# Kernel tuning notes

Measured on AMD Instinct MI355X. Metric: run time of the kernel, lower is better.

The kernel has to match this reference:

```python
import jax, jax.numpy as jnp
import numpy as np

B, T, N, F, C, H, O = 4, 8, 4096, 32, 32, 64, 1
RADIUS = 50.0   # adjacency_threshold on pairwise distance
EPS = 1e-5      # batchnorm eps


def setup_inputs() -> dict:
    key = jax.random.key(0)
    ks = jax.random.split(key, 8)
    x = jax.random.normal(ks[0], (B, T, N, F), jnp.float32)
    # dist_mat from random 2D node locations in a 1000x1000 area; avg degree ~32
    loc = jax.random.uniform(ks[1], (N, 2), jnp.float32) * 1000.0
    d2 = jnp.sum((loc[:, None, :] - loc[None, :, :]) ** 2, axis=-1)  # [N,N]
    adj = (d2 < RADIUS ** 2).astype(jnp.float32)                     # includes self (d=0)
    dinv = 1.0 / jnp.sqrt(jnp.maximum(adj.sum(-1), 1.0))
    adj_norm = adj * dinv[:, None] * dinv[None, :]                   # D^-1/2 A D^-1/2
    s = 0.05
    return dict(
        x=x,
        adj_norm=adj_norm,
        bn_gamma=jnp.ones((F,), jnp.float32),
        bn_beta=jnp.zeros((F,), jnp.float32),
        W_gcn=jax.random.normal(ks[2], (F, C), jnp.float32) * s,
        b_gcn=jnp.zeros((C,), jnp.float32),
        W_ih=jax.random.normal(ks[3], (C, 3 * H), jnp.float32) * s,
        W_hh=jax.random.normal(ks[4], (H, 3 * H), jnp.float32) * s,
        b_ih=jnp.zeros((3 * H,), jnp.float32),
        b_hh=jnp.zeros((3 * H,), jnp.float32),
        W_dense=jax.random.normal(ks[5], (H, O), jnp.float32) * s,
        b_dense=jnp.zeros((O,), jnp.float32),
    )


def reference(x, adj_norm, bn_gamma, bn_beta, W_gcn, b_gcn, W_ih, W_hh, b_ih, b_hh, W_dense, b_dense):
    # BatchNorm2d over feature channel (training-mode batch stats, biased var)
    mean = x.mean(axis=(0, 1, 2))
    var = x.var(axis=(0, 1, 2))
    xn = (x - mean) * jax.lax.rsqrt(var + EPS) * bn_gamma + bn_beta  # [B,T,N,F]
    # GCN association (same math every timestep -> batch over T)
    ya = jnp.einsum('mn,btnf->btmf', adj_norm, xn)                   # neighbor aggregate
    y = jnp.einsum('btnf,fc->btnc', ya, W_gcn) + b_gcn               # [B,T,N,C]
    # precompute input-gate projections, then scan GRU cell over time
    gi = jnp.einsum('btnc,ch->btnh', y, W_ih) + b_ih                 # [B,T,N,3H]
    gi = jnp.transpose(gi, (1, 0, 2, 3))                             # [T,B,N,3H]

    def step(h, g):
        gh = h @ W_hh + b_hh
        r = jax.nn.sigmoid(g[..., :H] + gh[..., :H])
        z = jax.nn.sigmoid(g[..., H:2 * H] + gh[..., H:2 * H])
        n = jnp.tanh(g[..., 2 * H:] + r * gh[..., 2 * H:])
        h_new = (1.0 - z) * n + z * h
        return h_new, h_new

    h0 = jnp.zeros((B, N, H), x.dtype)
    _, hs = jax.lax.scan(step, h0, gi)                               # [T,B,N,H]
    out = jnp.transpose(hs, (1, 0, 2, 3)) @ W_dense + b_dense        # [B,T,N,O]
    return out
```

## Files before the change

kernel.cpp:

```cpp
#include <hip/hip_runtime.h>
#include <hip/hip_bf16.h>
#include <stdint.h>

#define B_ 4
#define T_ 8
#define N_ 4096
#define F_ 32
#define BT_ (B_*T_)
#define ROWS_ (B_*N_)
#define CAP_ 128
#define EPS_ 1e-5f
#define NELEM_ (B_*T_*N_*F_)

#define WS_BNS    0
#define WS_ROWSUM 16384
#define WS_DEG    (WS_ROWSUM + 4096)
#define WS_FRG    (WS_DEG + 4096)
#define WS_PAIR   (WS_FRG + 52*256)
#define WS_XA     (WS_PAIR + 4096*CAP_*2)

typedef float v4f __attribute__((ext_vector_type(4)));
typedef _Float16 half8 __attribute__((ext_vector_type(8)));
union HU { uint32_t u[4]; half8 v; };

__device__ inline float sigm_f(float x) {
  return __builtin_amdgcn_rcpf(1.0f + __expf(-x));
}
__device__ inline uint32_t f16pair(float a, float b) {
  union { _Float16 h; unsigned short s; } x, y;
  x.h = (_Float16)a; y.h = (_Float16)b;
  return (uint32_t)x.s | ((uint32_t)y.s << 16);
}
__device__ inline void sp2(float a0, float a1, uint32_t& hi, uint32_t& lo) {
  _Float16 h0 = (_Float16)a0, h1 = (_Float16)a1;
  float r0 = a0 - (float)h0, r1 = a1 - (float)h1;
  union { _Float16 h; unsigned short s; } u0, u1, v0, v1;
  u0.h = h0; u1.h = h1; v0.h = (_Float16)r0; v1.h = (_Float16)r1;
  hi = (uint32_t)u0.s | ((uint32_t)u1.s << 16);
  lo = (uint32_t)v0.s | ((uint32_t)v1.s << 16);
}

__global__ void __launch_bounds__(256)
k_pre(const float* __restrict__ x, const float* __restrict__ A, float* __restrict__ ws) {
  if (blockIdx.x < 4096) {
    int m = blockIdx.x;
    __shared__ int cnt;
    __shared__ float wsum[4];
    if (threadIdx.x == 0) cnt = 0;
    __syncthreads();
    int* deg = (int*)&ws[WS_DEG];
    float2* pair = (float2*)&ws[WS_PAIR];
    const float4* A4 = (const float4*)(A + (size_t)m * N_);
    float4 av4[4];
#pragma unroll
    for (int i = 0; i < 4; i++) av4[i] = A4[threadIdx.x + 256 * i];
    float lsum = 0.f;
#pragma unroll
    for (int i = 0; i < 4; i++) {
      float av[4] = {av4[i].x, av4[i].y, av4[i].z, av4[i].w};
      int nb4 = (threadIdx.x + 256 * i) * 4;
#pragma unroll
      for (int r = 0; r < 4; r++) {
        float a = av[r];
        if (a != 0.0f) {
          int p = atomicAdd(&cnt, 1);
          if (p < CAP_) pair[(size_t)m * CAP_ + p] = make_float2(__int_as_float((nb4 + r) * F_), a);
          lsum += a;
        }
      }
    }
#pragma unroll
    for (int off = 32; off > 0; off >>= 1) lsum += __shfl_xor(lsum, off, 64);
    if ((threadIdx.x & 63) == 0) wsum[threadIdx.x >> 6] = lsum;
    __syncthreads();
    int c = cnt;
    for (int p = c + threadIdx.x; p < 68; p += 256)
      pair[(size_t)m * CAP_ + p] = make_float2(__int_as_float(0), 0.0f);
    if (threadIdx.x == 0) {
      deg[m] = min(c, CAP_);
      ws[WS_ROWSUM + m] = wsum[0] + wsum[1] + wsum[2] + wsum[3];
    }
  } else {
    int bnb = blockIdx.x - 4096;
    const float4* x4 = (const float4*)x;
    int tid = bnb * 256 + threadIdx.x;
    float s[4] = {0,0,0,0}, s2[4] = {0,0,0,0};
    for (int i = tid; i < NELEM_ / 4; i += 256 * 256) {
      float4 v = x4[i];
      s[0] += v.x; s2[0] += v.x * v.x;
      s[1] += v.y; s2[1] += v.y * v.y;
      s[2] += v.z; s2[2] += v.z * v.z;
      s[3] += v.w; s2[3] += v.w * v.w;
    }
    __shared__ float ls[256][4], ls2[256][4];
#pragma unroll
    for (int r = 0; r < 4; r++) { ls[threadIdx.x][r] = s[r]; ls2[threadIdx.x][r] = s2[r]; }
    __syncthreads();
    int t = threadIdx.x;
    if (t < 32) {
      int g = t >> 2, r = t & 3;
      float a = 0.f;
      for (int q = g; q < 256; q += 8) a += ls[q][r];
      atomicAdd(&ws[WS_BNS + t], a);
    } else if (t < 64) {
      int cch = t - 32;
      int g = cch >> 2, r = cch & 3;
      float b2 = 0.f;
      for (int q = g; q < 256; q += 8) b2 += ls2[q][r];
      atomicAdd(&ws[WS_BNS + t], b2);
    }
  }
}

__global__ void __launch_bounds__(256)
k_fold(const float* __restrict__ gamma, const float* __restrict__ beta,
       const float* __restrict__ Wg, const float* __restrict__ bg,
       const float* __restrict__ Wih, const float* __restrict__ bih,
       const float* __restrict__ Whh, const float* __restrict__ bhh,
       float* __restrict__ ws) {
  __shared__ float fb[26144];
  float* Wx_s  = fb;
  float* Wih_s = fb + 6144;
  float* Whh_s = fb + 12288;
  float* Wg_s  = fb + 24576;
  float* Us_s  = fb + 25600;
  float* Vs_s  = fb + 25792;
  float* bns   = fb + 25984;
  float* scale_s = fb + 26048;
  float* shift_s = fb + 26080;
  float* p_s   = fb + 26112;
  int tid = threadIdx.x;
#pragma unroll
  for (int i = tid; i < 1536; i += 256) ((float4*)Wih_s)[i] = ((const float4*)Wih)[i];
#pragma unroll
  for (int i = tid; i < 3072; i += 256) ((float4*)Whh_s)[i] = ((const float4*)Whh)[i];
  if (tid < 256) { ((float4*)Wg_s)[tid] = ((const float4*)Wg)[tid]; }
  if (tid < 64) bns[tid] = ws[WS_BNS + tid];
  __syncthreads();
  if (tid < 32) {
    float cntf = (float)(B_ * T_ * N_);
    float mean = bns[tid] / cntf;
    float var = bns[32 + tid] / cntf - mean * mean;
    float sc = gamma[tid] * rsqrtf(var + EPS_);
    scale_s[tid] = sc;
    shift_s[tid] = beta[tid] - mean * sc;
  }
  __syncthreads();
  if (tid < 32) {
    float acc = 0.f;
    for (int f = 0; f < 32; f++) acc += shift_s[f] * Wg_s[f * 32 + tid];
    p_s[tid] = acc;
  }
  __syncthreads();
  for (int e = tid; e < 32 * 192; e += 256) {
    int f = e / 192, j = e % 192;
    float acc = 0.f;
#pragma unroll
    for (int c = 0; c < 32; c++) acc += Wg_s[f * 32 + c] * Wih_s[c * 192 + j];
    Wx_s[e] = scale_s[f] * acc;
  }
  if (tid < 192) {
    float au = 0.f, av = 0.f;
#pragma unroll
    for (int c = 0; c < 32; c++) { au += p_s[c] * Wih_s[c * 192 + tid]; av += bg[c] * Wih_s[c * 192 + tid]; }
    Us_s[tid] = au; Vs_s[tid] = av + bih[tid];
  }
  __syncthreads();
  int w = tid >> 6, L = tid & 63, q = L >> 4, c = L & 15;
  uint32_t* wsu = (uint32_t*)ws;
  for (int fi = w; fi < 52; fi += 4) {
    int mt, kt;
    if (fi < 32)      { mt = fi >> 2;            kt = fi & 3; }
    else if (fi < 40) { mt = 8 + ((fi - 32) >> 1); kt = (fi & 1) ? 3 : 0; }
    else              { int r = fi - 40; mt = 12 + r / 3; kt = 1 + r % 3; }
    int cls = mt >> 2;
    int col = (cls < 2) ? mt * 16 + c : 128 + (mt & 3) * 16 + c;
#pragma unroll
    for (int d = 0; d < 4; d++) {
      float a01[2];
#pragma unroll
      for (int h2 = 0; h2 < 2; h2++) {
        int k = kt * 32 + q * 8 + 2 * d + h2;
        float v;
        if (k < 32)       v = (cls == 3) ? 0.f : Wx_s[k * 192 + col];
        else if (k < 96)  v = (cls == 2) ? 0.f : Whh_s[(k - 32) * 192 + col];
        else if (k == 96) v = (cls == 3) ? 0.f : Us_s[col];
        else if (k == 97) v = (cls < 2) ? (Vs_s[col] + bhh[col]) : (cls == 2 ? Vs_s[col] : bhh[col]);
        else              v = 0.f;
        a01[h2] = v;
      }
      wsu[WS_FRG + fi * 256 + L * 4 + d] = f16pair(a01[0], a01[1]);
    }
  }
}

#define AGG_STEP(d) { \
    float vv = pv[d]; \
    v4f t0 = pb0[d], t1 = pb1[d]; \
    float2 p = pl[row * 69 + k + 4 + d]; \
    int off = __float_as_int(p.x) + fo; \
    pv[d] = p.y; \
    pb0[d] = *(const v4f*)(xb0 + off); \
    pb1[d] = *(const v4f*)(xb1 + off); \
    acc0 += vv * t0; acc1 += vv * t1; }

__global__ void __launch_bounds__(256, 8)
k_agg(const float* __restrict__ x, float* __restrict__ ws) {
  __shared__ float2 pl[32 * 69];
  int tid = threadIdx.x;
  int chunk = blockIdx.x & 15;
  int mg = blockIdx.x >> 4;
  int row = tid >> 3, f4 = tid & 7;
  int m = mg * 32 + row;
  const int* deg = (const int*)&ws[WS_DEG];
  const float2* pair = (const float2*)&ws[WS_PAIR];
  for (int qq = tid; qq < 32 * 68; qq += 256) {
    int r = qq / 68, sl = qq - r * 68;
    pl[r * 69 + sl] = pair[(size_t)(mg * 32 + r) * CAP_ + sl];
  }
  __syncthreads();
  int d0 = deg[m];
  int dm = min(d0, 64);
  int bound = dm;
  bound = max(bound, __shfl_xor(bound, 8, 64));
  bound = max(bound, __shfl_xor(bound, 16, 64));
  bound = max(bound, __shfl_xor(bound, 32, 64));
  bound = (bound + 3) & ~3;
  int bt0 = chunk * 2;
  const float* xb0 = x + (size_t)bt0 * N_ * F_;
  const float* xb1 = xb0 + N_ * F_;
  int fo = f4 * 4;
  v4f acc0 = {0,0,0,0}, acc1 = {0,0,0,0};
  v4f pb0[4], pb1[4];
  float pv[4];
#pragma unroll
  for (int d = 0; d < 4; d++) {
    float2 p = pl[row * 69 + d];
    int off = __float_as_int(p.x) + fo;
    pv[d] = p.y;
    pb0[d] = *(const v4f*)(xb0 + off);
    pb1[d] = *(const v4f*)(xb1 + off);
  }
  for (int k = 0; k < bound; k += 4) {
    AGG_STEP(0) AGG_STEP(1) AGG_STEP(2) AGG_STEP(3)
  }
  if (d0 > 64) {
    for (int k = 64; k < d0; k++) {
      float2 p = pair[(size_t)m * CAP_ + k];
      int off = __float_as_int(p.x) + fo;
      float vv = p.y;
      acc0 += vv * *(const v4f*)(xb0 + off);
      acc1 += vv * *(const v4f*)(xb1 + off);
    }
  }
  size_t ob = (size_t)bt0 * N_ * F_ + m * F_ + fo;
  *(v4f*)(ws + WS_XA + ob) = acc0;
  *(v4f*)(ws + WS_XA + ob + (size_t)N_ * F_) = acc1;
}

#define LDA(fi) (*(const half8*)(frg + (fi)*256 + L*4))
#define DO1(mt, fi, BH, BL) { half8 af = LDA(fi); \
  acc[mt] = __builtin_amdgcn_mfma_f32_16x16x32_f16(af, BH, acc[mt], 0, 0, 0); \
  acc[mt] = __builtin_amdgcn_mfma_f32_16x16x32_f16(af, BL, acc[mt], 0, 0, 0); }

__global__ void __launch_bounds__(256, 1)
k_gru(const float* __restrict__ Wd, const float* __restrict__ bd,
      const float* __restrict__ ws, float* __restrict__ out) {
  __shared__ uint32_t frg[52 * 256];
  __shared__ uint32_t hx[4 * 1344];
  {
    const uint4* gf = (const uint4*)(ws + WS_FRG);
    uint4* sf = (uint4*)frg;
    for (int i = threadIdx.x; i < 52 * 64; i += 256) sf[i] = gf[i];
  }
  __syncthreads();
  int wid = threadIdx.x >> 6, L = threadIdx.x & 63;
  int q = L >> 4, c = L & 15;
  uint32_t* hxw = hx + wid * 1344;
  int row0 = blockIdx.x * 64 + wid * 16;
  int b = row0 >> 12;
  int nb = row0 & (N_ - 1);
  float wdv[4][4];
#pragma unroll
  for (int g = 0; g < 4; g++)
#pragma unroll
    for (int r = 0; r < 4; r++) wdv[g][r] = Wd[16 * g + 4 * q + r];
  float bdv = bd[0];
  HU b3h, b3l;
#pragma unroll
  for (int d = 0; d < 4; d++) { b3h.u[d] = 0; b3l.u[d] = 0; }
  {
    float rsv = ws[WS_ROWSUM + nb + c];
    uint32_t rhi, rlo;
    sp2(rsv, 1.0f, rhi, rlo);
    if (q == 0) { b3h.u[0] = rhi; b3l.u[0] = rlo & 0xFFFFu; }
  }
  float h[4][4];
#pragma unroll
  for (int g = 0; g < 4; g++)
#pragma unroll
    for (int r = 0; r < 4; r++) h[g][r] = 0.f;

  const float* xab = ws + WS_XA;
  size_t xo0 = ((size_t)(b * T_) * N_ + nb + c) * F_ + q * 8;
  float4 xaA = *(const float4*)(xab + xo0);
  float4 xaB = *(const float4*)(xab + xo0 + 4);

  for (int t = 0; t < T_; t++) {
    float4 nxA, nxB;
    if (t < T_ - 1) {
      size_t xo = ((size_t)(b * T_ + t + 1) * N_ + nb + c) * F_ + q * 8;
      nxA = *(const float4*)(xab + xo);
      nxB = *(const float4*)(xab + xo + 4);
    }
#pragma unroll
    for (int g = 0; g < 4; g++)
#pragma unroll
      for (int rp = 0; rp < 2; rp++) {
        uint32_t phi, plo;
        sp2(h[g][2 * rp], h[g][2 * rp + 1], phi, plo);
        int pidx = 8 * g + 2 * q + rp;
        hxw[(pidx * 2 + 0) * 21 + c] = phi;
        hxw[(pidx * 2 + 1) * 21 + c] = plo;
      }
    HU b1h, b1l, b2h, b2l;
#pragma unroll
    for (int d = 0; d < 4; d++) {
      b1h.u[d] = hxw[((4 * q + d) * 2 + 0) * 21 + c];
      b1l.u[d] = hxw[((4 * q + d) * 2 + 1) * 21 + c];
      b2h.u[d] = hxw[((16 + 4 * q + d) * 2 + 0) * 21 + c];
      b2l.u[d] = hxw[((16 + 4 * q + d) * 2 + 1) * 21 + c];
    }
    v4f acc[16];
#pragma unroll
    for (int i = 0; i < 16; i++) acc[i] = (v4f){0.f, 0.f, 0.f, 0.f};
    DO1(0,1,b1h.v,b1l.v)  DO1(1,5,b1h.v,b1l.v)  DO1(2,9,b1h.v,b1l.v)  DO1(3,13,b1h.v,b1l.v)
    DO1(4,17,b1h.v,b1l.v) DO1(5,21,b1h.v,b1l.v) DO1(6,25,b1h.v,b1l.v) DO1(7,29,b1h.v,b1l.v)
    DO1(12,40,b1h.v,b1l.v) DO1(13,43,b1h.v,b1l.v) DO1(14,46,b1h.v,b1l.v) DO1(15,49,b1h.v,b1l.v)
    DO1(0,2,b2h.v,b2l.v)  DO1(1,6,b2h.v,b2l.v)  DO1(2,10,b2h.v,b2l.v) DO1(3,14,b2h.v,b2l.v)
    DO1(4,18,b2h.v,b2l.v) DO1(5,22,b2h.v,b2l.v) DO1(6,26,b2h.v,b2l.v) DO1(7,30,b2h.v,b2l.v)
    DO1(12,41,b2h.v,b2l.v) DO1(13,44,b2h.v,b2l.v) DO1(14,47,b2h.v,b2l.v) DO1(15,50,b2h.v,b2l.v)
    DO1(0,3,b3h.v,b3l.v)  DO1(1,7,b3h.v,b3l.v)  DO1(2,11,b3h.v,b3l.v) DO1(3,15,b3h.v,b3l.v)
    DO1(4,19,b3h.v,b3l.v) DO1(5,23,b3h.v,b3l.v) DO1(6,27,b3h.v,b3l.v) DO1(7,31,b3h.v,b3l.v)
    DO1(8,33,b3h.v,b3l.v) DO1(9,35,b3h.v,b3l.v) DO1(10,37,b3h.v,b3l.v) DO1(11,39,b3h.v,b3l.v)
    DO1(12,42,b3h.v,b3l.v) DO1(13,45,b3h.v,b3l.v) DO1(14,48,b3h.v,b3l.v) DO1(15,51,b3h.v,b3l.v)
    HU b0h, b0l;
    sp2(xaA.x, xaA.y, b0h.u[0], b0l.u[0]);
    sp2(xaA.z, xaA.w, b0h.u[1], b0l.u[1]);
    sp2(xaB.x, xaB.y, b0h.u[2], b0l.u[2]);
    sp2(xaB.z, xaB.w, b0h.u[3], b0l.u[3]);
    DO1(0,0,b0h.v,b0l.v)  DO1(1,4,b0h.v,b0l.v)  DO1(2,8,b0h.v,b0l.v)  DO1(3,12,b0h.v,b0l.v)
    DO1(4,16,b0h.v,b0l.v) DO1(5,20,b0h.v,b0l.v) DO1(6,24,b0h.v,b0l.v) DO1(7,28,b0h.v,b0l.v)
    DO1(8,32,b0h.v,b0l.v) DO1(9,34,b0h.v,b0l.v) DO1(10,36,b0h.v,b0l.v) DO1(11,38,b0h.v,b0l.v)
    float o = 0.f;
#pragma unroll
    for (int g = 0; g < 4; g++)
#pragma unroll
      for (int r = 0; r < 4; r++) {
        float rr = sigm_f(acc[g][r]);
        float z  = sigm_f(acc[4 + g][r]);
        float nn = 2.0f * sigm_f(2.0f * (acc[8 + g][r] + rr * acc[12 + g][r])) - 1.0f;
        float hn = z * (h[g][r] - nn) + nn;
        h[g][r] = hn;
        o += wdv[g][r] * hn;
      }
    o += __shfl_xor(o, 16, 64);
    o += __shfl_xor(o, 32, 64);
    if (L < 16) out[(size_t)(b * T_ + t) * N_ + nb + L] = o + bdv;
    xaA = nxA; xaB = nxB;
  }
}

extern "C" void kernel_launch(void* const* d_in, const int* in_sizes, int n_in,
                              void* d_out, int out_size, void* d_ws, size_t ws_size,
                              hipStream_t stream) {
  const float* x     = (const float*)d_in[0];
  const float* adj   = (const float*)d_in[1];
  const float* gamma = (const float*)d_in[2];
  const float* beta  = (const float*)d_in[3];
  const float* Wg    = (const float*)d_in[4];
  const float* bg    = (const float*)d_in[5];
  const float* Wih   = (const float*)d_in[6];
  const float* Whh   = (const float*)d_in[7];
  const float* bih   = (const float*)d_in[8];
  const float* bhh   = (const float*)d_in[9];
  const float* Wd    = (const float*)d_in[10];
  const float* bd    = (const float*)d_in[11];
  float* ws = (float*)d_ws;
  float* out = (float*)d_out;

  hipMemsetAsync(ws + WS_BNS, 0, 64 * sizeof(float), stream);
  k_pre<<<4096 + 256, 256, 0, stream>>>(x, adj, ws);
  k_fold<<<1, 256, 0, stream>>>(gamma, beta, Wg, bg, Wih, bih, Whh, bhh, ws);
  k_agg<<<2048, 256, 0, stream>>>(x, ws);
  k_gru<<<256, 256, 0, stream>>>(Wd, bd, ws, out);
}
```

Baseline: 206.9 us.

## Fuse sparse neighbor aggregation into GRU kernel via shared memory

Removes the separate aggregation kernel and computes the neighbor-aggregated features for each block's 64 rows across all 8 timesteps directly inside the GRU kernel, keeping them in LDS. This avoids writing and re-reading the aggregated tensor through global memory and saves a kernel launch. In exchange, the gather now runs with only 256 blocks and one block per CU, so far fewer waves are available to hide the latency of the irregular loads. The neighbor-list buffer shares LDS with the hidden-state staging through a union.

```diff
diff --git a/kernel.cpp b/kernel.cpp
--- a/kernel.cpp
+++ b/kernel.cpp
@@ -17,7 +17,6 @@
 #define WS_DEG    (WS_ROWSUM + 4096)
 #define WS_FRG    (WS_DEG + 4096)
 #define WS_PAIR   (WS_FRG + 52*256)
-#define WS_XA     (WS_PAIR + 4096*CAP_*2)
 
 typedef float v4f __attribute__((ext_vector_type(4)));
 typedef _Float16 half8 __attribute__((ext_vector_type(8)));
@@ -194,92 +193,97 @@
   }
 }
 
-#define AGG_STEP(d) { \
-    float vv = pv[d]; \
-    v4f t0 = pb0[d], t1 = pb1[d]; \
-    float2 p = pl[row * 69 + k + 4 + d]; \
-    int off = __float_as_int(p.x) + fo; \
-    pv[d] = p.y; \
-    pb0[d] = *(const v4f*)(xb0 + off); \
-    pb1[d] = *(const v4f*)(xb1 + off); \
-    acc0 += vv * t0; acc1 += vv * t1; }
-
-__global__ void __launch_bounds__(256, 8)
-k_agg(const float* __restrict__ x, float* __restrict__ ws) {
-  __shared__ float2 pl[32 * 69];
-  int tid = threadIdx.x;
-  int chunk = blockIdx.x & 15;
-  int mg = blockIdx.x >> 4;
-  int row = tid >> 3, f4 = tid & 7;
-  int m = mg * 32 + row;
-  const int* deg = (const int*)&ws[WS_DEG];
-  const float2* pair = (const float2*)&ws[WS_PAIR];
-  for (int qq = tid; qq < 32 * 68; qq += 256) {
-    int r = qq / 68, sl = qq - r * 68;
-    pl[r * 69 + sl] = pair[(size_t)(mg * 32 + r) * CAP_ + sl];
-  }
-  __syncthreads();
-  int d0 = deg[m];
-  int dm = min(d0, 64);
-  int bound = dm;
-  bound = max(bound, __shfl_xor(bound, 8, 64));
-  bound = max(bound, __shfl_xor(bound, 16, 64));
-  bound = max(bound, __shfl_xor(bound, 32, 64));
-  bound = (bound + 3) & ~3;
-  int bt0 = chunk * 2;
-  const float* xb0 = x + (size_t)bt0 * N_ * F_;
-  const float* xb1 = xb0 + N_ * F_;
-  int fo = f4 * 4;
-  v4f acc0 = {0,0,0,0}, acc1 = {0,0,0,0};
-  v4f pb0[4], pb1[4];
-  float pv[4];
-#pragma unroll
-  for (int d = 0; d < 4; d++) {
-    float2 p = pl[row * 69 + d];
-    int off = __float_as_int(p.x) + fo;
-    pv[d] = p.y;
-    pb0[d] = *(const v4f*)(xb0 + off);
-    pb1[d] = *(const v4f*)(xb1 + off);
-  }
-  for (int k = 0; k < bound; k += 4) {
-    AGG_STEP(0) AGG_STEP(1) AGG_STEP(2) AGG_STEP(3)
-  }
-  if (d0 > 64) {
-    for (int k = 64; k < d0; k++) {
-      float2 p = pair[(size_t)m * CAP_ + k];
-      int off = __float_as_int(p.x) + fo;
-      float vv = p.y;
-      acc0 += vv * *(const v4f*)(xb0 + off);
-      acc1 += vv * *(const v4f*)(xb1 + off);
-    }
-  }
-  size_t ob = (size_t)bt0 * N_ * F_ + m * F_ + fo;
-  *(v4f*)(ws + WS_XA + ob) = acc0;
-  *(v4f*)(ws + WS_XA + ob + (size_t)N_ * F_) = acc1;
-}
-
 #define LDA(fi) (*(const half8*)(frg + (fi)*256 + L*4))
 #define DO1(mt, fi, BH, BL) { half8 af = LDA(fi); \
   acc[mt] = __builtin_amdgcn_mfma_f32_16x16x32_f16(af, BH, acc[mt], 0, 0, 0); \
   acc[mt] = __builtin_amdgcn_mfma_f32_16x16x32_f16(af, BL, acc[mt], 0, 0, 0); }
 
 __global__ void __launch_bounds__(256, 1)
-k_gru(const float* __restrict__ Wd, const float* __restrict__ bd,
+k_gru(const float* __restrict__ x, const float* __restrict__ Wd, const float* __restrict__ bd,
       const float* __restrict__ ws, float* __restrict__ out) {
   __shared__ uint32_t frg[52 * 256];
-  __shared__ uint32_t hx[4 * 1344];
+  __shared__ float xaF[8 * 64 * 34];
+  __shared__ union { float2 pl[64 * 72]; uint32_t hx[4 * 1344]; } u;
+  int tid = threadIdx.x;
   {
     const uint4* gf = (const uint4*)(ws + WS_FRG);
     uint4* sf = (uint4*)frg;
-    for (int i = threadIdx.x; i < 52 * 64; i += 256) sf[i] = gf[i];
-  }
-  __syncthreads();
-  int wid = threadIdx.x >> 6, L = threadIdx.x & 63;
+    for (int i = tid; i < 52 * 64; i += 256) sf[i] = gf[i];
+  }
+  int b = (blockIdx.x & 7) >> 1;
+  int nbb = (((blockIdx.x >> 3) << 1) | (blockIdx.x & 1)) * 64;
+  const float2* pair = (const float2*)&ws[WS_PAIR];
+  for (int qq = tid; qq < 64 * 72; qq += 256) {
+    int r = qq / 72, sl = qq - r * 72;
+    u.pl[r * 72 + sl] = (sl < 68) ? pair[(size_t)(nbb + r) * CAP_ + sl]
+                                  : make_float2(__int_as_float(0), 0.0f);
+  }
+  __syncthreads();
+
+  int wid = tid >> 6, L = tid & 63;
+  {
+    const int* deg = (const int*)&ws[WS_DEG];
+    int r8 = L >> 3, f4g = L & 7;
+    int fo = f4g * 4;
+    for (int sg = 0; sg < 2; sg++) {
+      int rloc = wid * 16 + sg * 8 + r8;
+      int d0 = deg[nbb + rloc];
+      int bound = min(d0, 64);
+      bound = max(bound, __shfl_xor(bound, 8, 64));
+      bound = max(bound, __shfl_xor(bound, 16, 64));
+      bound = max(bound, __shfl_xor(bound, 32, 64));
+      bound = (bound + 7) & ~7;
+      const float2* plr = u.pl + rloc * 72;
+#pragma unroll 1
+      for (int btp = 0; btp < 4; btp++) {
+        const float* xb0 = x + (size_t)(b * 8 + btp * 2) * N_ * F_;
+        const float* xb1 = xb0 + N_ * F_;
+        v4f acc0 = {0,0,0,0}, acc1 = {0,0,0,0};
+        v4f pb0[8], pb1[8];
+        float pv[8];
+#pragma unroll
+        for (int d = 0; d < 8; d++) {
+          float2 p = plr[d];
+          int off = __float_as_int(p.x) + fo;
+          pv[d] = p.y;
+          pb0[d] = *(const v4f*)(xb0 + off);
+          pb1[d] = *(const v4f*)(xb1 + off);
+        }
+        for (int k = 0; k < bound; k += 8) {
+#pragma unroll
+          for (int d = 0; d < 8; d++) {
+            float vv = pv[d];
+            v4f t0 = pb0[d], t1 = pb1[d];
+            float2 p = plr[k + 8 + d];
+            int off = __float_as_int(p.x) + fo;
+            pv[d] = p.y;
+            pb0[d] = *(const v4f*)(xb0 + off);
+            pb1[d] = *(const v4f*)(xb1 + off);
+            acc0 += vv * t0; acc1 += vv * t1;
+          }
+        }
+        if (d0 > 64) {
+          for (int k = 64; k < d0; k++) {
+            float2 p = pair[(size_t)(nbb + rloc) * CAP_ + k];
+            int off = __float_as_int(p.x) + fo;
+            acc0 += p.y * *(const v4f*)(xb0 + off);
+            acc1 += p.y * *(const v4f*)(xb1 + off);
+          }
+        }
+        int btl = btp * 2;
+        float* dst0 = &xaF[btl * 2176 + rloc * 34 + fo];
+        float* dst1 = dst0 + 2176;
+        *(float2*)dst0 = make_float2(acc0.x, acc0.y);
+        *(float2*)(dst0 + 2) = make_float2(acc0.z, acc0.w);
+        *(float2*)dst1 = make_float2(acc1.x, acc1.y);
+        *(float2*)(dst1 + 2) = make_float2(acc1.z, acc1.w);
+      }
+    }
+  }
+  __syncthreads();
+
   int q = L >> 4, c = L & 15;
-  uint32_t* hxw = hx + wid * 1344;
-  int row0 = blockIdx.x * 64 + wid * 16;
-  int b = row0 >> 12;
-  int nb = row0 & (N_ - 1);
+  uint32_t* hxw = u.hx + wid * 1344;
   float wdv[4][4];
 #pragma unroll
   for (int g = 0; g < 4; g++)
@@ -290,7 +294,7 @@
 #pragma unroll
   for (int d = 0; d < 4; d++) { b3h.u[d] = 0; b3l.u[d] = 0; }
   {
-    float rsv = ws[WS_ROWSUM + nb + c];
+    float rsv = ws[WS_ROWSUM + nbb + wid * 16 + c];
     uint32_t rhi, rlo;
     sp2(rsv, 1.0f, rhi, rlo);
     if (q == 0) { b3h.u[0] = rhi; b3l.u[0] = rlo & 0xFFFFu; }
@@ -301,18 +305,13 @@
 #pragma unroll
     for (int r = 0; r < 4; r++) h[g][r] = 0.f;
 
-  const float* xab = ws + WS_XA;
-  size_t xo0 = ((size_t)(b * T_) * N_ + nb + c) * F_ + q * 8;
-  float4 xaA = *(const float4*)(xab + xo0);
-  float4 xaB = *(const float4*)(xab + xo0 + 4);
-
+  int rowL = wid * 16 + c;
   for (int t = 0; t < T_; t++) {
-    float4 nxA, nxB;
-    if (t < T_ - 1) {
-      size_t xo = ((size_t)(b * T_ + t + 1) * N_ + nb + c) * F_ + q * 8;
-      nxA = *(const float4*)(xab + xo);
-      nxB = *(const float4*)(xab + xo + 4);
-    }
+    const float* xr = &xaF[t * 2176 + rowL * 34 + q * 8];
+    float2 a0 = *(const float2*)xr;
+    float2 a1 = *(const float2*)(xr + 2);
+    float2 a2 = *(const float2*)(xr + 4);
+    float2 a3 = *(const float2*)(xr + 6);
 #pragma unroll
     for (int g = 0; g < 4; g++)
 #pragma unroll
@@ -345,10 +344,10 @@
     DO1(8,33,b3h.v,b3l.v) DO1(9,35,b3h.v,b3l.v) DO1(10,37,b3h.v,b3l.v) DO1(11,39,b3h.v,b3l.v)
     DO1(12,42,b3h.v,b3l.v) DO1(13,45,b3h.v,b3l.v) DO1(14,48,b3h.v,b3l.v) DO1(15,51,b3h.v,b3l.v)
     HU b0h, b0l;
-    sp2(xaA.x, xaA.y, b0h.u[0], b0l.u[0]);
-    sp2(xaA.z, xaA.w, b0h.u[1], b0l.u[1]);
-    sp2(xaB.x, xaB.y, b0h.u[2], b0l.u[2]);
-    sp2(xaB.z, xaB.w, b0h.u[3], b0l.u[3]);
+    sp2(a0.x, a0.y, b0h.u[0], b0l.u[0]);
+    sp2(a1.x, a1.y, b0h.u[1], b0l.u[1]);
+    sp2(a2.x, a2.y, b0h.u[2], b0l.u[2]);
+    sp2(a3.x, a3.y, b0h.u[3], b0l.u[3]);
     DO1(0,0,b0h.v,b0l.v)  DO1(1,4,b0h.v,b0l.v)  DO1(2,8,b0h.v,b0l.v)  DO1(3,12,b0h.v,b0l.v)
     DO1(4,16,b0h.v,b0l.v) DO1(5,20,b0h.v,b0l.v) DO1(6,24,b0h.v,b0l.v) DO1(7,28,b0h.v,b0l.v)
     DO1(8,32,b0h.v,b0l.v) DO1(9,34,b0h.v,b0l.v) DO1(10,36,b0h.v,b0l.v) DO1(11,38,b0h.v,b0l.v)
@@ -366,8 +365,7 @@
       }
     o += __shfl_xor(o, 16, 64);
     o += __shfl_xor(o, 32, 64);
-    if (L < 16) out[(size_t)(b * T_ + t) * N_ + nb + L] = o + bdv;
-    xaA = nxA; xaB = nxB;
+    if (L < 16) out[(size_t)(b * T_ + t) * N_ + nbb + wid * 16 + L] = o + bdv;
   }
 }
 
@@ -392,6 +390,5 @@
   hipMemsetAsync(ws + WS_BNS, 0, 64 * sizeof(float), stream);
   k_pre<<<4096 + 256, 256, 0, stream>>>(x, adj, ws);
   k_fold<<<1, 256, 0, stream>>>(gamma, beta, Wg, bg, Wih, bih, Whh, bhh, ws);
-  k_agg<<<2048, 256, 0, stream>>>(x, ws);
-  k_gru<<<256, 256, 0, stream>>>(Wd, bd, ws, out);
-}
+  k_gru<<<256, 256, 0, stream>>>(x, Wd, bd, ws, out);
+}
```

Result: slower. 217.2 us (+4.9%).
